# Optimization experiments

Measured on AMD Instinct MI355X. Metric: run time of the kernel, lower is better.

The kernel has to match this reference:

```python
import jax, jax.numpy as jnp
import numpy as np

B, C, H, W = 16, 128, 56, 56
K = 3
F = K * K          # number of deformation filters = kernel taps
OUT = 512
STRIDE = 1


def setup_inputs() -> dict:
    key = jax.random.key(0)
    k1, k2, k3, k4 = jax.random.split(key, 4)
    x = jax.random.normal(k1, (B, C, H, W), jnp.float32)
    # Deform2d 1x1 offset conv: weight [2F, C], bias [2F] initialized to kernel tap offsets
    w_off = jax.random.normal(k2, (2 * F, C), jnp.float32) * 0.01
    half = K // 2
    xs = [float(dx) for dy in range(-half, K - half) for dx in range(-half, K - half)]
    ys = [float(dy) for dy in range(-half, K - half) for dx in range(-half, K - half)]
    b_off = jnp.array(xs + ys, jnp.float32)  # all x offsets first, then all y offsets
    # final 1x1 conv: [OUT, F*C]
    w_conv = jax.random.normal(k3, (OUT, F * C), jnp.float32) * (1.0 / np.sqrt(F * C))
    b_conv = jax.random.normal(k4, (OUT,), jnp.float32) * 0.01
    return {"x": x, "w_off": w_off, "b_off": b_off, "w_conv": w_conv, "b_conv": b_conv}


def _bilinear_sample(img, gx, gy):
    # img: [C,H,W]; gx, gy: [H,W] normalized coords in [-1,1]
    # torch grid_sample defaults: bilinear, zeros padding, align_corners=False
    C_, H_, W_ = img.shape
    ix = ((gx + 1.0) * W_ - 1.0) * 0.5
    iy = ((gy + 1.0) * H_ - 1.0) * 0.5
    x0 = jnp.floor(ix)
    y0 = jnp.floor(iy)
    wx1 = ix - x0
    wx0 = 1.0 - wx1
    wy1 = iy - y0
    wy0 = 1.0 - wy1

    def gather(yy, xx):
        valid = ((xx >= 0) & (xx < W_) & (yy >= 0) & (yy < H_)).astype(img.dtype)
        xi = jnp.clip(xx, 0, W_ - 1).astype(jnp.int32)
        yi = jnp.clip(yy, 0, H_ - 1).astype(jnp.int32)
        return img[:, yi, xi] * valid[None]  # [C,H,W]

    return (gather(y0, x0) * (wy0 * wx0)[None]
            + gather(y0, x0 + 1.0) * (wy0 * wx1)[None]
            + gather(y0 + 1.0, x0) * (wy1 * wx0)[None]
            + gather(y0 + 1.0, x0 + 1.0) * (wy1 * wx1)[None])


def reference(x, w_off, b_off, w_conv, b_conv):
    Bv, Cv, Hv, Wv = x.shape
    scale = 2.0 / max(Hv, Wv)
    # Deform2d: 1x1 conv -> per-pixel offsets, scaled to normalized grid units
    deform = (jnp.einsum('bchw,dc->bdhw', x, w_off) + b_off[None, :, None, None]) * scale
    # matches torch view(B*F, 2, H, W): consecutive channel pairs per filter
    deform = deform.reshape(Bv, F, 2, Hv, Wv)
    # identity grid from affine_grid (align_corners=False)
    base_x = (2.0 * jnp.arange(Wv, dtype=x.dtype) + 1.0) / Wv - 1.0
    base_y = (2.0 * jnp.arange(Hv, dtype=x.dtype) + 1.0) / Hv - 1.0
    # grid is detached in the torch code -> no gradient to the offset conv
    gx = jax.lax.stop_gradient(base_x[None, None, None, :] + deform[:, :, 0])  # [B,F,H,W]
    gy = jax.lax.stop_gradient(base_y[None, None, :, None] + deform[:, :, 1])  # [B,F,H,W]
    sample_f = jax.vmap(_bilinear_sample, in_axes=(None, 0, 0))   # over F filters (input shared)
    sample_bf = jax.vmap(sample_f, in_axes=(0, 0, 0))             # over batch
    sampled = sample_bf(x, gx, gy)                                 # [B,F,C,H,W]
    sampled = sampled.reshape(Bv, F * Cv, Hv, Wv)[:, :, ::STRIDE, ::STRIDE]
    # final 1x1 conv
    return jnp.einsum('bchw,oc->bohw', sampled, w_conv) + b_conv[None, :, None, None]
```

## Files before the change

kernel.cpp:

```cpp
#include <hip/hip_runtime.h>
#include <stdint.h>
#include <stddef.h>

#define BN 16
#define CN 128
#define HN 56
#define WN 56
#define HWN 3136
#define FN 9
#define DN 18
#define ON 512
#define KN 1152
#define MN 50176

typedef __bf16 bf16x8 __attribute__((ext_vector_type(8)));
typedef float f32x4 __attribute__((ext_vector_type(4)));

__device__ __forceinline__ unsigned short f2bf(float f) {
  unsigned int u = __builtin_bit_cast(unsigned int, f);
  u += 0x7fffu + ((u >> 16) & 1u);
  return (unsigned short)(u >> 16);
}

__device__ __forceinline__ void gload_lds16(const void* g, void* l) {
  __builtin_amdgcn_global_load_lds(
      (const __attribute__((address_space(1))) unsigned int*)g,
      (__attribute__((address_space(3))) unsigned int*)l, 16, 0, 0);
}

__global__ void k_transpose(const float* __restrict__ x, float* __restrict__ xt) {
  __shared__ float tile[32][33];
  const int b = blockIdx.z;
  const int hw0 = blockIdx.x * 32;
  const int c0 = blockIdx.y * 32;
  const int tx = threadIdx.x & 31;
  const int ty = threadIdx.x >> 5;
  const float* xb = x + (size_t)b * CN * HWN;
  float* xtb = xt + (size_t)b * HWN * CN;
#pragma unroll
  for (int r = 0; r < 4; ++r)
    tile[ty + r * 8][tx] = xb[(size_t)(c0 + ty + r * 8) * HWN + hw0 + tx];
  __syncthreads();
#pragma unroll
  for (int r = 0; r < 4; ++r)
    xtb[(size_t)(hw0 + ty + r * 8) * CN + c0 + tx] = tile[tx][ty + r * 8];
}

__global__ void k_wconv(const float4* __restrict__ w, ushort4* __restrict__ wb) {
  const int i = blockIdx.x * 256 + threadIdx.x;
  float4 v = w[i];
  ushort4 o;
  o.x = f2bf(v.x); o.y = f2bf(v.y); o.z = f2bf(v.z); o.w = f2bf(v.w);
  wb[i] = o;
}

__global__ void k_offsets(const float* __restrict__ xt, const float* __restrict__ w_off,
                          const float* __restrict__ b_off, float2* __restrict__ ixy) {
  const int m = blockIdx.x * 256 + threadIdx.x;
  const int b = m / HWN;
  const int hw = m - b * HWN;
  const int h = hw / WN;
  const int w = hw - h * WN;
  (void)b;
  const float* xp = xt + (size_t)m * CN;
  float acc[DN];
#pragma unroll
  for (int d = 0; d < DN; ++d) acc[d] = b_off[d];
  for (int c = 0; c < CN; c += 4) {
    float4 xv = *(const float4*)(xp + c);
#pragma unroll
    for (int d = 0; d < DN; ++d) {
      const float* wr = w_off + d * CN + c;
      acc[d] += xv.x * wr[0] + xv.y * wr[1] + xv.z * wr[2] + xv.w * wr[3];
    }
  }
  const float scale = 2.0f / 56.0f;
  const float bx = (2.0f * w + 1.0f) / (float)WN - 1.0f;
  const float by = (2.0f * h + 1.0f) / (float)HN - 1.0f;
#pragma unroll
  for (int f = 0; f < FN; ++f) {
    float gx = bx + acc[2 * f] * scale;
    float gy = by + acc[2 * f + 1] * scale;
    float ixv = ((gx + 1.0f) * (float)WN - 1.0f) * 0.5f;
    float iyv = ((gy + 1.0f) * (float)HN - 1.0f) * 0.5f;
    ixy[(size_t)m * FN + f] = make_float2(ixv, iyv);
  }
}

__global__ void k_sample(const float* __restrict__ xt, const float2* __restrict__ ixy,
                         unsigned short* __restrict__ S) {
  const int g = blockIdx.x * 256 + threadIdx.x;
  const int cc = g & 15;
  const int mf = g >> 4;
  const int m = mf / FN;
  const int f = mf - m * FN;
  const int b = m / HWN;

  const float2 p = ixy[mf];
  const float ix = p.x, iy = p.y;
  const float x0f = floorf(ix), y0f = floorf(iy);
  const float wx1 = ix - x0f, wy1 = iy - y0f;
  const float wx0 = 1.0f - wx1, wy0 = 1.0f - wy1;
  const int x0 = (int)x0f, y0 = (int)y0f;
  const int x1 = x0 + 1, y1 = y0 + 1;
  const bool vx0 = (x0 >= 0) & (x0 < WN), vx1 = (x1 >= 0) & (x1 < WN);
  const bool vy0 = (y0 >= 0) & (y0 < HN), vy1 = (y1 >= 0) & (y1 < HN);
  const float w00 = wy0 * wx0 * ((vy0 & vx0) ? 1.0f : 0.0f);
  const float w01 = wy0 * wx1 * ((vy0 & vx1) ? 1.0f : 0.0f);
  const float w10 = wy1 * wx0 * ((vy1 & vx0) ? 1.0f : 0.0f);
  const float w11 = wy1 * wx1 * ((vy1 & vx1) ? 1.0f : 0.0f);
  const int x0c = min(max(x0, 0), WN - 1), x1c = min(max(x1, 0), WN - 1);
  const int y0c = min(max(y0, 0), HN - 1), y1c = min(max(y1, 0), HN - 1);

  const float* bp = xt + (size_t)b * HWN * CN + cc * 8;
  const float4* p00 = (const float4*)(bp + (size_t)(y0c * WN + x0c) * CN);
  const float4* p01 = (const float4*)(bp + (size_t)(y0c * WN + x1c) * CN);
  const float4* p10 = (const float4*)(bp + (size_t)(y1c * WN + x0c) * CN);
  const float4* p11 = (const float4*)(bp + (size_t)(y1c * WN + x1c) * CN);
  float4 a0 = p00[0], a1 = p00[1];
  float4 b0 = p01[0], b1 = p01[1];
  float4 c0 = p10[0], c1 = p10[1];
  float4 d0 = p11[0], d1 = p11[1];

  float o0 = w00 * a0.x + w01 * b0.x + w10 * c0.x + w11 * d0.x;
  float o1 = w00 * a0.y + w01 * b0.y + w10 * c0.y + w11 * d0.y;
  float o2 = w00 * a0.z + w01 * b0.z + w10 * c0.z + w11 * d0.z;
  float o3 = w00 * a0.w + w01 * b0.w + w10 * c0.w + w11 * d0.w;
  float o4 = w00 * a1.x + w01 * b1.x + w10 * c1.x + w11 * d1.x;
  float o5 = w00 * a1.y + w01 * b1.y + w10 * c1.y + w11 * d1.y;
  float o6 = w00 * a1.z + w01 * b1.z + w10 * c1.z + w11 * d1.z;
  float o7 = w00 * a1.w + w01 * b1.w + w10 * c1.w + w11 * d1.w;

  uint4 ov;
  ov.x = (unsigned)f2bf(o0) | ((unsigned)f2bf(o1) << 16);
  ov.y = (unsigned)f2bf(o2) | ((unsigned)f2bf(o3) << 16);
  ov.z = (unsigned)f2bf(o4) | ((unsigned)f2bf(o5) << 16);
  ov.w = (unsigned)f2bf(o6) | ((unsigned)f2bf(o7) << 16);
  *(uint4*)(S + (size_t)m * KN + f * CN + cc * 8) = ov;
}

__global__ __launch_bounds__(256) void k_gemm(const unsigned short* __restrict__ Wb,
                                              const unsigned short* __restrict__ S,
                                              const float* __restrict__ bias,
                                              float* __restrict__ out) {
  __shared__ __align__(16) unsigned short lw[128 * 32];
  __shared__ __align__(16) unsigned short ls[128 * 32];
  const int tid = threadIdx.x;
  const int wave = tid >> 6;
  const int lane = tid & 63;
  const int quad = lane >> 4;
  const int r16 = lane & 15;
  const int p0 = blockIdx.x * 128;
  const int o0 = blockIdx.y * 128;
  const int wrow = wave >> 1;
  const int wcol = wave & 1;

  f32x4 acc[4][4];
#pragma unroll
  for (int i = 0; i < 4; ++i)
#pragma unroll
    for (int j = 0; j < 4; ++j) acc[i][j] = (f32x4){0.f, 0.f, 0.f, 0.f};

  const int srow = tid >> 2;
  const int scol = (tid & 3) * 8;
  const unsigned short* gw0 = Wb + (size_t)(o0 + srow) * KN + scol;
  const unsigned short* gw1 = Wb + (size_t)(o0 + 64 + srow) * KN + scol;
  const unsigned short* gs0 = S + (size_t)(p0 + srow) * KN + scol;
  const unsigned short* gs1 = S + (size_t)(p0 + 64 + srow) * KN + scol;
  unsigned short* lwd = lw + wave * 512;
  unsigned short* lsd = ls + wave * 512;

  const unsigned short* aw = lw + (wrow * 64 + r16) * 32 + quad * 8;
  const unsigned short* bs = ls + (wcol * 64 + r16) * 32 + quad * 8;

  for (int kt = 0; kt < KN / 32; ++kt) {
    gload_lds16(gw0, lwd);
    gload_lds16(gw1, lwd + 2048);
    gload_lds16(gs0, lsd);
    gload_lds16(gs1, lsd + 2048);
    gw0 += 32; gw1 += 32; gs0 += 32; gs1 += 32;
    __syncthreads();
    bf16x8 afr[4], bfr[4];
#pragma unroll
    for (int i = 0; i < 4; ++i) afr[i] = *(const bf16x8*)(aw + i * 16 * 32);
#pragma unroll
    for (int j = 0; j < 4; ++j) bfr[j] = *(const bf16x8*)(bs + j * 16 * 32);
#pragma unroll
    for (int i = 0; i < 4; ++i)
#pragma unroll
      for (int j = 0; j < 4; ++j)
        acc[i][j] = __builtin_amdgcn_mfma_f32_16x16x32_bf16(afr[i], bfr[j], acc[i][j], 0, 0, 0);
    __syncthreads();
  }

#pragma unroll
  for (int i = 0; i < 4; ++i) {
    const int o = o0 + wrow * 64 + i * 16 + quad * 4;
    const float b0v = bias[o], b1v = bias[o + 1], b2v = bias[o + 2], b3v = bias[o + 3];
#pragma unroll
    for (int j = 0; j < 4; ++j) {
      const int p = p0 + wcol * 64 + j * 16 + r16;
      const int bidx = p / HWN;
      const int hw = p - bidx * HWN;
      float* op = out + (size_t)bidx * ON * HWN + hw;
      op[(size_t)(o + 0) * HWN] = acc[i][j][0] + b0v;
      op[(size_t)(o + 1) * HWN] = acc[i][j][1] + b1v;
      op[(size_t)(o + 2) * HWN] = acc[i][j][2] + b2v;
      op[(size_t)(o + 3) * HWN] = acc[i][j][3] + b3v;
    }
  }
}

extern "C" void kernel_launch(void* const* d_in, const int* in_sizes, int n_in,
                              void* d_out, int out_size, void* d_ws, size_t ws_size,
                              hipStream_t stream) {
  const float* x = (const float*)d_in[0];
  const float* w_off = (const float*)d_in[1];
  const float* b_off = (const float*)d_in[2];
  const float* w_conv = (const float*)d_in[3];
  const float* b_conv = (const float*)d_in[4];
  float* out = (float*)d_out;

  char* ws = (char*)d_ws;
  float* xt = (float*)(ws);
  unsigned short* S = (unsigned short*)(ws + 25690112);
  unsigned short* Wb = (unsigned short*)(ws + 141295616);
  float2* ixy = (float2*)(ws + 142475264);

  k_transpose<<<dim3(98, 4, 16), 256, 0, stream>>>(x, xt);
  k_wconv<<<dim3(576), 256, 0, stream>>>((const float4*)w_conv, (ushort4*)Wb);
  k_offsets<<<dim3(196), 256, 0, stream>>>(xt, w_off, b_off, ixy);
  k_sample<<<dim3(28224), 256, 0, stream>>>(xt, ixy, S);
  k_gemm<<<dim3(392, 4), 256, 0, stream>>>(Wb, S, b_conv, out);
}
```

Baseline: 294.2 us.

## Store transposed input in bf16, widen GEMM k-tile with swizzled LDS, stage epilogue

The transposed input is stored as bf16, which halves the traffic for the offset conv and the bilinear gather, and each sampling thread now handles 16 channels. The GEMM k-step grows from 32 to 64 with an XOR swizzle on the LDS layout to avoid bank conflicts. The output tile is staged through LDS so the stores become coalesced float4 writes. The grid is swapped so the four output-channel blocks sharing a pixel tile run next to each other for L2 reuse. Offsets are now computed from bf16-rounded inputs, which adds a small accuracy risk.

```diff
diff --git a/kernel.cpp b/kernel.cpp
--- a/kernel.cpp
+++ b/kernel.cpp
@@ -28,7 +28,7 @@
       (__attribute__((address_space(3))) unsigned int*)l, 16, 0, 0);
 }
 
-__global__ void k_transpose(const float* __restrict__ x, float* __restrict__ xt) {
+__global__ void k_transpose(const float* __restrict__ x, unsigned short* __restrict__ xt) {
   __shared__ float tile[32][33];
   const int b = blockIdx.z;
   const int hw0 = blockIdx.x * 32;
@@ -36,14 +36,14 @@
   const int tx = threadIdx.x & 31;
   const int ty = threadIdx.x >> 5;
   const float* xb = x + (size_t)b * CN * HWN;
-  float* xtb = xt + (size_t)b * HWN * CN;
+  unsigned short* xtb = xt + (size_t)b * HWN * CN;
 #pragma unroll
   for (int r = 0; r < 4; ++r)
     tile[ty + r * 8][tx] = xb[(size_t)(c0 + ty + r * 8) * HWN + hw0 + tx];
   __syncthreads();
 #pragma unroll
   for (int r = 0; r < 4; ++r)
-    xtb[(size_t)(hw0 + ty + r * 8) * CN + c0 + tx] = tile[tx][ty + r * 8];
+    xtb[(size_t)(hw0 + ty + r * 8) * CN + c0 + tx] = f2bf(tile[tx][ty + r * 8]);
 }
 
 __global__ void k_wconv(const float4* __restrict__ w, ushort4* __restrict__ wb) {
@@ -54,24 +54,27 @@
   wb[i] = o;
 }
 
-__global__ void k_offsets(const float* __restrict__ xt, const float* __restrict__ w_off,
+__global__ void k_offsets(const unsigned short* __restrict__ xt, const float* __restrict__ w_off,
                           const float* __restrict__ b_off, float2* __restrict__ ixy) {
   const int m = blockIdx.x * 256 + threadIdx.x;
   const int b = m / HWN;
   const int hw = m - b * HWN;
   const int h = hw / WN;
   const int w = hw - h * WN;
-  (void)b;
-  const float* xp = xt + (size_t)m * CN;
+  const unsigned short* xp = xt + (size_t)m * CN;
   float acc[DN];
 #pragma unroll
   for (int d = 0; d < DN; ++d) acc[d] = b_off[d];
-  for (int c = 0; c < CN; c += 4) {
-    float4 xv = *(const float4*)(xp + c);
+  for (int c = 0; c < CN; c += 8) {
+    bf16x8 xv = *(const bf16x8*)(xp + c);
+    float xf[8];
+#pragma unroll
+    for (int q = 0; q < 8; ++q) xf[q] = (float)xv[q];
 #pragma unroll
     for (int d = 0; d < DN; ++d) {
       const float* wr = w_off + d * CN + c;
-      acc[d] += xv.x * wr[0] + xv.y * wr[1] + xv.z * wr[2] + xv.w * wr[3];
+#pragma unroll
+      for (int q = 0; q < 8; ++q) acc[d] += xf[q] * wr[q];
     }
   }
   const float scale = 2.0f / 56.0f;
@@ -87,11 +90,11 @@
   }
 }
 
-__global__ void k_sample(const float* __restrict__ xt, const float2* __restrict__ ixy,
+__global__ void k_sample(const unsigned short* __restrict__ xt, const float2* __restrict__ ixy,
                          unsigned short* __restrict__ S) {
   const int g = blockIdx.x * 256 + threadIdx.x;
-  const int cc = g & 15;
-  const int mf = g >> 4;
+  const int cc = g & 7;
+  const int mf = g >> 3;
   const int m = mf / FN;
   const int f = mf - m * FN;
   const int b = m / HWN;
@@ -112,46 +115,43 @@
   const int x0c = min(max(x0, 0), WN - 1), x1c = min(max(x1, 0), WN - 1);
   const int y0c = min(max(y0, 0), HN - 1), y1c = min(max(y1, 0), HN - 1);
 
-  const float* bp = xt + (size_t)b * HWN * CN + cc * 8;
-  const float4* p00 = (const float4*)(bp + (size_t)(y0c * WN + x0c) * CN);
-  const float4* p01 = (const float4*)(bp + (size_t)(y0c * WN + x1c) * CN);
-  const float4* p10 = (const float4*)(bp + (size_t)(y1c * WN + x0c) * CN);
-  const float4* p11 = (const float4*)(bp + (size_t)(y1c * WN + x1c) * CN);
-  float4 a0 = p00[0], a1 = p00[1];
-  float4 b0 = p01[0], b1 = p01[1];
-  float4 c0 = p10[0], c1 = p10[1];
-  float4 d0 = p11[0], d1 = p11[1];
-
-  float o0 = w00 * a0.x + w01 * b0.x + w10 * c0.x + w11 * d0.x;
-  float o1 = w00 * a0.y + w01 * b0.y + w10 * c0.y + w11 * d0.y;
-  float o2 = w00 * a0.z + w01 * b0.z + w10 * c0.z + w11 * d0.z;
-  float o3 = w00 * a0.w + w01 * b0.w + w10 * c0.w + w11 * d0.w;
-  float o4 = w00 * a1.x + w01 * b1.x + w10 * c1.x + w11 * d1.x;
-  float o5 = w00 * a1.y + w01 * b1.y + w10 * c1.y + w11 * d1.y;
-  float o6 = w00 * a1.z + w01 * b1.z + w10 * c1.z + w11 * d1.z;
-  float o7 = w00 * a1.w + w01 * b1.w + w10 * c1.w + w11 * d1.w;
-
-  uint4 ov;
-  ov.x = (unsigned)f2bf(o0) | ((unsigned)f2bf(o1) << 16);
-  ov.y = (unsigned)f2bf(o2) | ((unsigned)f2bf(o3) << 16);
-  ov.z = (unsigned)f2bf(o4) | ((unsigned)f2bf(o5) << 16);
-  ov.w = (unsigned)f2bf(o6) | ((unsigned)f2bf(o7) << 16);
-  *(uint4*)(S + (size_t)m * KN + f * CN + cc * 8) = ov;
+  const unsigned short* bp = xt + (size_t)b * HWN * CN + cc * 16;
+  const bf16x8* p00 = (const bf16x8*)(bp + (size_t)(y0c * WN + x0c) * CN);
+  const bf16x8* p01 = (const bf16x8*)(bp + (size_t)(y0c * WN + x1c) * CN);
+  const bf16x8* p10 = (const bf16x8*)(bp + (size_t)(y1c * WN + x0c) * CN);
+  const bf16x8* p11 = (const bf16x8*)(bp + (size_t)(y1c * WN + x1c) * CN);
+  bf16x8 a0 = p00[0], a1 = p00[1];
+  bf16x8 b0 = p01[0], b1 = p01[1];
+  bf16x8 c0 = p10[0], c1 = p10[1];
+  bf16x8 d0 = p11[0], d1 = p11[1];
+
+  unsigned short ov[16];
+#pragma unroll
+  for (int q = 0; q < 8; ++q) {
+    float lo = w00 * (float)a0[q] + w01 * (float)b0[q] + w10 * (float)c0[q] + w11 * (float)d0[q];
+    float hi = w00 * (float)a1[q] + w01 * (float)b1[q] + w10 * (float)c1[q] + w11 * (float)d1[q];
+    ov[q] = f2bf(lo);
+    ov[q + 8] = f2bf(hi);
+  }
+  uint4* dst = (uint4*)(S + (size_t)m * KN + f * CN + cc * 16);
+  dst[0] = *(const uint4*)(ov);
+  dst[1] = *(const uint4*)(ov + 8);
 }
 
 __global__ __launch_bounds__(256) void k_gemm(const unsigned short* __restrict__ Wb,
                                               const unsigned short* __restrict__ S,
                                               const float* __restrict__ bias,
                                               float* __restrict__ out) {
-  __shared__ __align__(16) unsigned short lw[128 * 32];
-  __shared__ __align__(16) unsigned short ls[128 * 32];
+  __shared__ __align__(16) char smem[32768];
+  unsigned short* lw = (unsigned short*)smem;
+  unsigned short* ls = (unsigned short*)(smem + 16384);
   const int tid = threadIdx.x;
   const int wave = tid >> 6;
   const int lane = tid & 63;
   const int quad = lane >> 4;
   const int r16 = lane & 15;
-  const int p0 = blockIdx.x * 128;
-  const int o0 = blockIdx.y * 128;
+  const int o0 = blockIdx.x * 128;
+  const int p0 = blockIdx.y * 128;
   const int wrow = wave >> 1;
   const int wcol = wave & 1;
 
@@ -161,52 +161,75 @@
 #pragma unroll
     for (int j = 0; j < 4; ++j) acc[i][j] = (f32x4){0.f, 0.f, 0.f, 0.f};
 
-  const int srow = tid >> 2;
-  const int scol = (tid & 3) * 8;
-  const unsigned short* gw0 = Wb + (size_t)(o0 + srow) * KN + scol;
-  const unsigned short* gw1 = Wb + (size_t)(o0 + 64 + srow) * KN + scol;
-  const unsigned short* gs0 = S + (size_t)(p0 + srow) * KN + scol;
-  const unsigned short* gs1 = S + (size_t)(p0 + 64 + srow) * KN + scol;
+  const int row0 = tid >> 3;
+  const int swc = (((tid & 7) ^ (row0 & 7))) * 8;
+  const unsigned short* gw = Wb + (size_t)(o0 + row0) * KN + swc;
+  const unsigned short* gs = S + (size_t)(p0 + row0) * KN + swc;
   unsigned short* lwd = lw + wave * 512;
   unsigned short* lsd = ls + wave * 512;
 
-  const unsigned short* aw = lw + (wrow * 64 + r16) * 32 + quad * 8;
-  const unsigned short* bs = ls + (wcol * 64 + r16) * 32 + quad * 8;
-
-  for (int kt = 0; kt < KN / 32; ++kt) {
-    gload_lds16(gw0, lwd);
-    gload_lds16(gw1, lwd + 2048);
-    gload_lds16(gs0, lsd);
-    gload_lds16(gs1, lsd + 2048);
-    gw0 += 32; gw1 += 32; gs0 += 32; gs1 += 32;
-    __syncthreads();
-    bf16x8 afr[4], bfr[4];
-#pragma unroll
-    for (int i = 0; i < 4; ++i) afr[i] = *(const bf16x8*)(aw + i * 16 * 32);
-#pragma unroll
-    for (int j = 0; j < 4; ++j) bfr[j] = *(const bf16x8*)(bs + j * 16 * 32);
-#pragma unroll
-    for (int i = 0; i < 4; ++i)
-#pragma unroll
-      for (int j = 0; j < 4; ++j)
-        acc[i][j] = __builtin_amdgcn_mfma_f32_16x16x32_bf16(afr[i], bfr[j], acc[i][j], 0, 0, 0);
-    __syncthreads();
-  }
-
-#pragma unroll
-  for (int i = 0; i < 4; ++i) {
-    const int o = o0 + wrow * 64 + i * 16 + quad * 4;
-    const float b0v = bias[o], b1v = bias[o + 1], b2v = bias[o + 2], b3v = bias[o + 3];
-#pragma unroll
-    for (int j = 0; j < 4; ++j) {
-      const int p = p0 + wcol * 64 + j * 16 + r16;
+  const int rsw = r16 & 7;
+  const int ch0 = (quad ^ rsw) * 8;
+  const int ch1 = ((quad ^ rsw) ^ 4) * 8;
+  const unsigned short* aw = lw + (wrow * 64 + r16) * 64;
+  const unsigned short* bs = ls + (wcol * 64 + r16) * 64;
+
+  for (int kt = 0; kt < KN / 64; ++kt) {
+#pragma unroll
+    for (int r = 0; r < 4; ++r) {
+      gload_lds16(gw + (size_t)r * 32 * KN, lwd + r * 2048);
+      gload_lds16(gs + (size_t)r * 32 * KN, lsd + r * 2048);
+    }
+    gw += 64; gs += 64;
+    __syncthreads();
+#pragma unroll
+    for (int h = 0; h < 2; ++h) {
+      const int ch = h ? ch1 : ch0;
+      bf16x8 afr[4], bfr[4];
+#pragma unroll
+      for (int i = 0; i < 4; ++i) afr[i] = *(const bf16x8*)(aw + i * 16 * 64 + ch);
+#pragma unroll
+      for (int j = 0; j < 4; ++j) bfr[j] = *(const bf16x8*)(bs + j * 16 * 64 + ch);
+#pragma unroll
+      for (int i = 0; i < 4; ++i)
+#pragma unroll
+        for (int j = 0; j < 4; ++j)
+          acc[i][j] = __builtin_amdgcn_mfma_f32_16x16x32_bf16(afr[i], bfr[j], acc[i][j], 0, 0, 0);
+    }
+    __syncthreads();
+  }
+
+  float* lout = (float*)smem;
+  for (int half = 0; half < 2; ++half) {
+    __syncthreads();
+    if (wrow == half) {
+#pragma unroll
+      for (int i = 0; i < 4; ++i) {
+        const int orow = i * 16 + quad * 4;
+#pragma unroll
+        for (int j = 0; j < 4; ++j) {
+          const int col = wcol * 64 + j * 16 + r16;
+          lout[(orow + 0) * 128 + col] = acc[i][j][0];
+          lout[(orow + 1) * 128 + col] = acc[i][j][1];
+          lout[(orow + 2) * 128 + col] = acc[i][j][2];
+          lout[(orow + 3) * 128 + col] = acc[i][j][3];
+        }
+      }
+    }
+    __syncthreads();
+#pragma unroll
+    for (int t = 0; t < 8; ++t) {
+      const int idx = t * 256 + tid;
+      const int orow = idx >> 5;
+      const int c4 = idx & 31;
+      float4 v = ((const float4*)lout)[idx];
+      const int o = o0 + half * 64 + orow;
+      const float bv = bias[o];
+      v.x += bv; v.y += bv; v.z += bv; v.w += bv;
+      const int p = p0 + c4 * 4;
       const int bidx = p / HWN;
       const int hw = p - bidx * HWN;
-      float* op = out + (size_t)bidx * ON * HWN + hw;
-      op[(size_t)(o + 0) * HWN] = acc[i][j][0] + b0v;
-      op[(size_t)(o + 1) * HWN] = acc[i][j][1] + b1v;
-      op[(size_t)(o + 2) * HWN] = acc[i][j][2] + b2v;
-      op[(size_t)(o + 3) * HWN] = acc[i][j][3] + b3v;
+      *(float4*)(out + (size_t)bidx * ON * HWN + (size_t)o * HWN + hw) = v;
     }
   }
 }
@@ -222,14 +245,14 @@
   float* out = (float*)d_out;
 
   char* ws = (char*)d_ws;
-  float* xt = (float*)(ws);
-  unsigned short* S = (unsigned short*)(ws + 25690112);
-  unsigned short* Wb = (unsigned short*)(ws + 141295616);
-  float2* ixy = (float2*)(ws + 142475264);
+  unsigned short* xt = (unsigned short*)(ws);
+  unsigned short* S = (unsigned short*)(ws + 12845056);
+  unsigned short* Wb = (unsigned short*)(ws + 128450560);
+  float2* ixy = (float2*)(ws + 129630208);
 
   k_transpose<<<dim3(98, 4, 16), 256, 0, stream>>>(x, xt);
   k_wconv<<<dim3(576), 256, 0, stream>>>((const float4*)w_conv, (ushort4*)Wb);
   k_offsets<<<dim3(196), 256, 0, stream>>>(xt, w_off, b_off, ixy);
-  k_sample<<<dim3(28224), 256, 0, stream>>>(xt, ixy, S);
-  k_gemm<<<dim3(392, 4), 256, 0, stream>>>(Wb, S, b_conv, out);
-}
+  k_sample<<<dim3(14112), 256, 0, stream>>>(xt, ixy, S);
+  k_gemm<<<dim3(4, 392), 256, 0, stream>>>(Wb, S, b_conv, out);
+}
```

Result: faster. 269.7 us (-8.3%).
